# Kernel tuning notes

Measured on AMD Instinct MI355X. Metric: run time of the kernel, lower is better.

Reference implementation:

```python
import jax, jax.numpy as jnp
import numpy as np

D_MODEL = 1024
N_HEADS = 16
D_K = D_MODEL // N_HEADS

def _xavier(key, shape):
    fan_in, fan_out = shape[1], shape[0]
    limit = float(np.sqrt(6.0 / (fan_in + fan_out)))
    return jax.random.uniform(key, shape, jnp.float32, -limit, limit)

def setup_inputs() -> dict:
    key = jax.random.key(0)
    ks = jax.random.split(key, 7)
    B, S = 2, 2048
    return {
        "query": jax.random.normal(ks[0], (B, S, D_MODEL), jnp.float32),
        "key": jax.random.normal(ks[1], (B, S, D_MODEL), jnp.float32),
        "value": jax.random.normal(ks[2], (B, S, D_MODEL), jnp.float32),
        "w_q": _xavier(ks[3], (D_MODEL, D_MODEL)),  # torch Linear weight [out, in]
        "w_k": _xavier(ks[4], (D_MODEL, D_MODEL)),
        "w_v": _xavier(ks[5], (D_MODEL, D_MODEL)),
        "w_o": _xavier(ks[6], (D_MODEL, D_MODEL)),
        "ln_gamma": jnp.ones((D_MODEL,), jnp.float32),
        "ln_beta": jnp.zeros((D_MODEL,), jnp.float32),
    }

def reference(query, key, value, w_q, w_k, w_v, w_o, ln_gamma, ln_beta):
    B, S, _ = query.shape
    # projections (torch Linear: x @ W.T), split into heads -> [B, H, S, d_k]
    def split_heads(x, W):
        return (x @ W.T).reshape(B, S, N_HEADS, D_K).transpose(0, 2, 1, 3)
    Q = split_heads(query, w_q)
    K = split_heads(key, w_k)
    V = split_heads(value, w_v)
    scores = jnp.einsum('bhqd,bhkd->bhqk', Q, K) / jnp.sqrt(jnp.float32(D_K))
    attn = jax.nn.softmax(scores, axis=-1)  # dropout disabled (p=0 / eval)
    ctx = jnp.einsum('bhqk,bhkd->bhqd', attn, V)
    ctx = ctx.transpose(0, 2, 1, 3).reshape(B, S, D_MODEL)
    out = ctx @ w_o.T
    # residual + LayerNorm
    x = query + out
    mu = jnp.mean(x, axis=-1, keepdims=True)
    var = jnp.var(x, axis=-1, keepdims=True)
    return (x - mu) / jnp.sqrt(var + 1e-5) * ln_gamma + ln_beta
```

## Files before the change

### kernel.cpp

```cpp
#include <hip/hip_runtime.h>
#include <hip/hip_bf16.h>

#define DEVI __device__ __forceinline__

typedef float f32x4 __attribute__((ext_vector_type(4)));
typedef short bf16x8 __attribute__((ext_vector_type(8)));
typedef unsigned short ushort_t;

DEVI ushort_t f2bf(float x) {
  union { float f; unsigned u; } c; c.f = x;
  unsigned u = c.u;
  unsigned r = (u + 0x7fffu + ((u >> 16) & 1u)) >> 16;
  return (ushort_t)r;
}

DEVI float bf2f(unsigned hw) {
  union { unsigned u; float f; } c; c.u = hw << 16; return c.f;
}

DEVI unsigned cvt_pk_bf16(float lo, float hi) {
  unsigned r;
  asm volatile("v_cvt_pk_bf16_f32 %0, %1, %2" : "=v"(r) : "v"(lo), "v"(hi));
  return r;
}

DEVI void gload16(const ushort_t* g, ushort_t* l) {
  __builtin_amdgcn_global_load_lds(
      (const __attribute__((address_space(1))) unsigned int*)g,
      (__attribute__((address_space(3))) unsigned int*)l, 16, 0, 0);
}

#define WAITL0() asm volatile("s_waitcnt lgkmcnt(0)" ::: "memory")


__global__ __launch_bounds__(256)
void cvtN_kernel(const float* __restrict__ p0, const float* __restrict__ p1,
                 const float* __restrict__ p2, const float* __restrict__ p3,
                 ushort_t* __restrict__ o0, ushort_t* __restrict__ o1,
                 ushort_t* __restrict__ o2, ushort_t* __restrict__ o3, int n8) {
  int z = blockIdx.y;
  const float* in = (z == 0) ? p0 : (z == 1) ? p1 : (z == 2) ? p2 : p3;
  ushort_t* out = (z == 0) ? o0 : (z == 1) ? o1 : (z == 2) ? o2 : o3;
  int i = blockIdx.x * 256 + threadIdx.x;
  if (i >= n8) return;
  const float4* p = (const float4*)in + (size_t)i * 2;
  float4 a = p[0], b = p[1];
  uint4 v;
  v.x = cvt_pk_bf16(a.x, a.y);
  v.y = cvt_pk_bf16(a.z, a.w);
  v.z = cvt_pk_bf16(b.x, b.y);
  v.w = cvt_pk_bf16(b.z, b.w);
  ((uint4*)out)[i] = v;
}


__global__ __launch_bounds__(256)
void gemm128(const ushort_t* __restrict__ A0, const ushort_t* __restrict__ A1,
             const ushort_t* __restrict__ A2,
             const ushort_t* __restrict__ W0, const ushort_t* __restrict__ W1,
             const ushort_t* __restrict__ W2,
             void* __restrict__ O0, void* __restrict__ O1,
             void* __restrict__ O2, int mode_base, int nsteps, float qscale) {
  constexpr int K = 1024;
  int z = blockIdx.z;
  int mode = (mode_base == 3) ? 3 : mode_base + z;
  const ushort_t* A = (z == 0) ? A0 : (z == 1) ? A1 : A2;
  const ushort_t* W = (z == 0) ? W0 : (z == 1) ? W1 : W2;
  void* Op = (z == 0) ? O0 : (z == 1) ? O1 : O2;
  if (mode == 3) {
    A = A0 + z * 512;
    W = W0 + z * 512;
    Op = z ? O1 : O0;
  }
  float scale = (mode == 0) ? qscale : 1.0f;
  int m0 = (mode == 2) ? blockIdx.x * 128 : blockIdx.y * 128;
  int n0 = (mode == 2) ? blockIdx.y * 128 : blockIdx.x * 128;

  __shared__ __align__(16) ushort_t Asm[2][128 * 64];
  __shared__ __align__(16) ushort_t Bsm[2][128 * 64];

  int t = threadIdx.x;
  int lane = t & 63, wave = t >> 6;
  int wm = wave >> 1, wn = wave & 1;
  int col = lane & 15, g = lane >> 4;
  int lr = lane >> 3, lc = lane & 7;
  int cswz = col & 7;

  const ushort_t* aSrc = A + (size_t)(m0 + wave * 32 + lr) * K + (lc ^ lr) * 8;
  const ushort_t* bSrc = W + (size_t)(n0 + wave * 32 + lr) * K + (lc ^ lr) * 8;

  f32x4 z4 = {0.f, 0.f, 0.f, 0.f};
  f32x4 acc[4][4];
  for (int i = 0; i < 4; i++)
    for (int j = 0; j < 4; j++) acc[i][j] = z4;

#define GEMM_STAGE(buf, koff) do {                                         \
    _Pragma("unroll")                                                      \
    for (int i_ = 0; i_ < 4; i_++) {                                       \
      gload16(aSrc + (koff) + i_ * 8 * K,                                  \
              &Asm[buf][(wave * 32 + i_ * 8) * 64]);                       \
      gload16(bSrc + (koff) + i_ * 8 * K,                                  \
              &Bsm[buf][(wave * 32 + i_ * 8) * 64]);                       \
    }                                                                      \
  } while (0)

  GEMM_STAGE(0, 0);
  __syncthreads();

  for (int kt = 0; kt < nsteps; ++kt) {
    int cur = kt & 1;
    if (kt < nsteps - 1) GEMM_STAGE(cur ^ 1, (kt + 1) * 64);
    const ushort_t* As = Asm[cur];
    const ushort_t* Bs = Bsm[cur];
#pragma unroll
    for (int kk = 0; kk < 2; ++kk) {
      bf16x8 af[4], bfr[4];
#pragma unroll
      for (int mi = 0; mi < 4; mi++) {
        int row = wm * 64 + mi * 16 + col;
        af[mi] = *(const bf16x8*)(As + row * 64 + (((kk * 4 + g) ^ cswz) * 8));
      }
#pragma unroll
      for (int ni = 0; ni < 4; ni++) {
        int row = wn * 64 + ni * 16 + col;
        bfr[ni] = *(const bf16x8*)(Bs + row * 64 + (((kk * 4 + g) ^ cswz) * 8));
      }
      __builtin_amdgcn_s_setprio(1);
#pragma unroll
      for (int mi = 0; mi < 4; mi++)
#pragma unroll
        for (int ni = 0; ni < 4; ni++)
          acc[mi][ni] = __builtin_amdgcn_mfma_f32_16x16x32_bf16(af[mi], bfr[ni],
                                                                acc[mi][ni], 0, 0, 0);
      __builtin_amdgcn_s_setprio(0);
    }
    __syncthreads();
  }

#pragma unroll
  for (int mi = 0; mi < 4; mi++)
#pragma unroll
    for (int ni = 0; ni < 4; ni++)
#pragma unroll
      for (int r = 0; r < 4; r++) {
        int m = m0 + wm * 64 + mi * 16 + g * 4 + r;
        int n = n0 + wn * 64 + ni * 16 + col;
        float v = acc[mi][ni][r] * scale;
        if (mode <= 1) {
          int b = m >> 11, s = m & 2047, h = n >> 6, d = n & 63;
          ((ushort_t*)Op)[(((size_t)(b * 16 + h) * 2048 + s) * 64) + d] = f2bf(v);
        } else if (mode == 2) {
          int h = m >> 6, d = m & 63, b = n >> 11, s = n & 2047;
          ((ushort_t*)Op)[(((size_t)(b * 16 + h) * 64 + d) * 2048) + s] = f2bf(v);
        } else {
          ((ushort_t*)Op)[(size_t)m * 1024 + n] = f2bf(v);
        }
      }
#undef GEMM_STAGE
}


__global__ __launch_bounds__(256, 4)
void attn_kernel(const ushort_t* __restrict__ Qh, const ushort_t* __restrict__ Kh,
                 const ushort_t* __restrict__ Vt, ushort_t* __restrict__ ctx) {
  int qt = blockIdx.x;
  int bh = blockIdx.y;
  int t = threadIdx.x, lane = t & 63, wave = t >> 6;
  int col = lane & 15, g = lane >> 4;
  int lr = lane >> 3, lc = lane & 7;
  int cswz = col & 7;
  int q0 = qt * 128 + wave * 32;

  const ushort_t* Qp = Qh + (size_t)bh * 2048 * 64;
  const ushort_t* Kp = Kh + (size_t)bh * 2048 * 64;
  const ushort_t* Vp = Vt + (size_t)bh * 64 * 2048;

  __shared__ __align__(16) ushort_t Ksm[2][64 * 64];
  __shared__ __align__(16) ushort_t Vsm[2][64 * 64];

  int slot0 = wave * 16 + lr;
  int slot1 = slot0 + 8;
  int key0 = (slot0 & 0x20) | ((slot0 & 0x0C) << 1) | ((slot0 & 0x10) >> 2) | (slot0 & 3);
  int key1 = (slot1 & 0x20) | ((slot1 & 0x0C) << 1) | ((slot1 & 0x10) >> 2) | (slot1 & 3);

  const ushort_t* kSrc0 = Kp + (size_t)key0 * 64 + (lc ^ lr) * 8;
  const ushort_t* kSrc1 = Kp + (size_t)key1 * 64 + (lc ^ lr) * 8;
  const ushort_t* vSrc = Vp + (size_t)(wave * 16 + lr) * 2048 + (lc ^ lr) * 8;

#define ATTN_STAGE(buf, k0) do { \
    gload16(kSrc0 + (size_t)(k0) * 64, &Ksm[buf][wave * 1024]);        \
    gload16(kSrc1 + (size_t)(k0) * 64, &Ksm[buf][wave * 1024 + 512]);  \
    gload16(vSrc + (k0),               &Vsm[buf][wave * 1024]);        \
    gload16(vSrc + (k0) + 16384,       &Vsm[buf][wave * 1024 + 512]);  \
  } while (0)

  bf16x8 qa0 = *(const bf16x8*)(Qp + (size_t)(q0 + col) * 64 + g * 8);
  bf16x8 qa1 = *(const bf16x8*)(Qp + (size_t)(q0 + col) * 64 + 32 + g * 8);
  bf16x8 qb0 = *(const bf16x8*)(Qp + (size_t)(q0 + 16 + col) * 64 + g * 8);
  bf16x8 qb1 = *(const bf16x8*)(Qp + (size_t)(q0 + 16 + col) * 64 + 32 + g * 8);

  f32x4 z4 = {0.f, 0.f, 0.f, 0.f};
  f32x4 oa[4], ob[4];
  for (int i = 0; i < 4; i++) { oa[i] = z4; ob[i] = z4; }
  f32x4 la = z4, lb = z4;

  ATTN_STAGE(0, 0);
  __syncthreads();

  for (int it = 0; it < 32; ++it) {
    int cur = it & 1;
    if (it < 31) ATTN_STAGE(cur ^ 1, (it + 1) * 64);

    const ushort_t* Ks = Ksm[cur];
    const ushort_t* Vs = Vsm[cur];

    f32x4 sa[4], sb[4];
#pragma unroll
    for (int kt = 0; kt < 4; kt++) {
      int off = (kt * 16 + col) * 64 + ((g ^ cswz) * 8);
      bf16x8 kf0 = *(const bf16x8*)(Ks + off);
      bf16x8 kf1 = *(const bf16x8*)(Ks + (off ^ 32));
      f32x4 a = z4, b = z4;
      __builtin_amdgcn_s_setprio(1);
      a = __builtin_amdgcn_mfma_f32_16x16x32_bf16(kf0, qa0, a, 0, 0, 0);
      a = __builtin_amdgcn_mfma_f32_16x16x32_bf16(kf1, qa1, a, 0, 0, 0);
      b = __builtin_amdgcn_mfma_f32_16x16x32_bf16(kf0, qb0, b, 0, 0, 0);
      b = __builtin_amdgcn_mfma_f32_16x16x32_bf16(kf1, qb1, b, 0, 0, 0);
      __builtin_amdgcn_s_setprio(0);
      sa[kt] = a; sb[kt] = b;
    }

    unsigned pka[8], pkb[8];
#pragma unroll
    for (int kt = 0; kt < 4; kt++) {
      float a0 = __builtin_amdgcn_exp2f(sa[kt][0]);
      float a1 = __builtin_amdgcn_exp2f(sa[kt][1]);
      float a2 = __builtin_amdgcn_exp2f(sa[kt][2]);
      float a3 = __builtin_amdgcn_exp2f(sa[kt][3]);
      la[0] += a0; la[1] += a1; la[2] += a2; la[3] += a3;
      pka[2 * kt]     = cvt_pk_bf16(a0, a1);
      pka[2 * kt + 1] = cvt_pk_bf16(a2, a3);
      float b0 = __builtin_amdgcn_exp2f(sb[kt][0]);
      float b1 = __builtin_amdgcn_exp2f(sb[kt][1]);
      float b2 = __builtin_amdgcn_exp2f(sb[kt][2]);
      float b3 = __builtin_amdgcn_exp2f(sb[kt][3]);
      lb[0] += b0; lb[1] += b1; lb[2] += b2; lb[3] += b3;
      pkb[2 * kt]     = cvt_pk_bf16(b0, b1);
      pkb[2 * kt + 1] = cvt_pk_bf16(b2, b3);
    }

#pragma unroll
    for (int kk = 0; kk < 2; kk++) {
      union { uint4 u; bf16x8 f; } ua, ub;
      ua.u.x = pka[4 * kk];     ua.u.y = pka[4 * kk + 1];
      ua.u.z = pka[4 * kk + 2]; ua.u.w = pka[4 * kk + 3];
      ub.u.x = pkb[4 * kk];     ub.u.y = pkb[4 * kk + 1];
      ub.u.z = pkb[4 * kk + 2]; ub.u.w = pkb[4 * kk + 3];
      __builtin_amdgcn_s_setprio(1);
#pragma unroll
      for (int dt = 0; dt < 4; dt++) {
        bf16x8 vf = *(const bf16x8*)(Vs + (dt * 16 + col) * 64 +
                                     (((kk * 4 + g) ^ cswz) * 8));
        oa[dt] = __builtin_amdgcn_mfma_f32_16x16x32_bf16(vf, ua.f, oa[dt], 0, 0, 0);
        ob[dt] = __builtin_amdgcn_mfma_f32_16x16x32_bf16(vf, ub.f, ob[dt], 0, 0, 0);
      }
      __builtin_amdgcn_s_setprio(0);
    }
    __syncthreads();
  }
#undef ATTN_STAGE

  float lva = (la[0] + la[1]) + (la[2] + la[3]);
  lva += __shfl_xor(lva, 16);
  lva += __shfl_xor(lva, 32);
  float lvb = (lb[0] + lb[1]) + (lb[2] + lb[3]);
  lvb += __shfl_xor(lvb, 16);
  lvb += __shfl_xor(lvb, 32);
  float inva = 1.0f / lva, invb = 1.0f / lvb;
  int b = bh >> 4, h = bh & 15;
#pragma unroll
  for (int dt = 0; dt < 4; dt++)
#pragma unroll
    for (int r = 0; r < 4; r++) {
      int d = dt * 16 + g * 4 + r;
      ctx[((size_t)(b * 2048 + q0 + col)) * 1024 + h * 64 + d] =
          f2bf(oa[dt][r] * inva);
      ctx[((size_t)(b * 2048 + q0 + 16 + col)) * 1024 + h * 64 + d] =
          f2bf(ob[dt][r] * invb);
    }
}


__global__ __launch_bounds__(256)
void ln_kernel(const float* __restrict__ resid, const ushort_t* __restrict__ p0,
               const ushort_t* __restrict__ p1,
               const float* __restrict__ gamma, const float* __restrict__ beta,
               float* __restrict__ out) {
  int m = blockIdx.x;
  int t = threadIdx.x;
  int lane = t & 63, wave = t >> 6;
  float4 a = ((const float4*)(resid + (size_t)m * 1024))[t];
  uint2 v0 = ((const uint2*)(p0 + (size_t)m * 1024))[t];
  uint2 v1 = ((const uint2*)(p1 + (size_t)m * 1024))[t];
  float4 x;
  x.x = a.x + bf2f(v0.x & 0xffffu) + bf2f(v1.x & 0xffffu);
  x.y = a.y + bf2f(v0.x >> 16)     + bf2f(v1.x >> 16);
  x.z = a.z + bf2f(v0.y & 0xffffu) + bf2f(v1.y & 0xffffu);
  x.w = a.w + bf2f(v0.y >> 16)     + bf2f(v1.y >> 16);
  float sum = (x.x + x.y) + (x.z + x.w);
  float ssq = x.x * x.x + x.y * x.y + x.z * x.z + x.w * x.w;
  for (int off = 1; off < 64; off <<= 1) {
    sum += __shfl_xor(sum, off);
    ssq += __shfl_xor(ssq, off);
  }
  __shared__ float red[8];
  if (lane == 0) { red[wave] = sum; red[4 + wave] = ssq; }
  __syncthreads();
  sum = red[0] + red[1] + red[2] + red[3];
  ssq = red[4] + red[5] + red[6] + red[7];
  float mu = sum * (1.f / 1024.f);
  float var = ssq * (1.f / 1024.f) - mu * mu;
  float rstd = rsqrtf(var + 1e-5f);
  const float4* gp = (const float4*)gamma;
  const float4* bp = (const float4*)beta;
  float4 gg = gp[t], bb = bp[t];
  float4 y;
  y.x = (x.x - mu) * rstd * gg.x + bb.x;
  y.y = (x.y - mu) * rstd * gg.y + bb.y;
  y.z = (x.z - mu) * rstd * gg.z + bb.z;
  y.w = (x.w - mu) * rstd * gg.w + bb.w;
  ((float4*)(out + (size_t)m * 1024))[t] = y;
}


extern "C" void kernel_launch(void* const* d_in, const int* in_sizes, int n_in,
                              void* d_out, int out_size, void* d_ws, size_t ws_size,
                              hipStream_t stream) {
  (void)in_sizes; (void)n_in; (void)out_size; (void)ws_size;
  const float* query = (const float*)d_in[0];
  const float* keyi  = (const float*)d_in[1];
  const float* value = (const float*)d_in[2];
  const float* w_q = (const float*)d_in[3];
  const float* w_k = (const float*)d_in[4];
  const float* w_v = (const float*)d_in[5];
  const float* w_o = (const float*)d_in[6];
  const float* ln_g = (const float*)d_in[7];
  const float* ln_b = (const float*)d_in[8];

  char* ws = (char*)d_ws;
  const size_t MB = 1u << 20;
  ushort_t* proj0 = (ushort_t*)(ws + 0 * MB);
  ushort_t* proj1 = (ushort_t*)(ws + 8 * MB);
  ushort_t* Xq  = (ushort_t*)(ws + 0 * MB);
  ushort_t* Xk  = (ushort_t*)(ws + 8 * MB);
  ushort_t* Xv  = (ushort_t*)(ws + 16 * MB);
  ushort_t* Wq  = (ushort_t*)(ws + 24 * MB);
  ushort_t* Wk  = (ushort_t*)(ws + 26 * MB);
  ushort_t* Wv  = (ushort_t*)(ws + 28 * MB);
  ushort_t* Wo  = (ushort_t*)(ws + 30 * MB);
  ushort_t* Qh  = (ushort_t*)(ws + 32 * MB);
  ushort_t* Kh  = (ushort_t*)(ws + 40 * MB);
  ushort_t* Vt  = (ushort_t*)(ws + 48 * MB);
  ushort_t* ctx = (ushort_t*)(ws + 56 * MB);

  const float SCL = 0.18033688f;

  cvtN_kernel<<<dim3(2048, 3), 256, 0, stream>>>(query, keyi, value, value,
                                                 Xq, Xk, Xv, Xv, 524288);
  cvtN_kernel<<<dim3(512, 4), 256, 0, stream>>>(w_q, w_k, w_v, w_o,
                                                Wq, Wk, Wv, Wo, 131072);

  gemm128<<<dim3(8, 32, 3), 256, 0, stream>>>(Xq, Xk, Wv, Wq, Wk, Xv,
                                              Qh, Kh, Vt, 0, 16, SCL);
  attn_kernel<<<dim3(16, 32), 256, 0, stream>>>(Qh, Kh, Vt, ctx);
  gemm128<<<dim3(8, 32, 2), 256, 0, stream>>>(ctx, ctx, ctx, Wo, Wo, Wo,
                                              proj0, proj1, proj0, 3, 8, 1.0f);
  ln_kernel<<<4096, 256, 0, stream>>>(query, proj0, proj1, ln_g, ln_b,
                                      (float*)d_out);
}
```

Measured before the change: 140.2 us.

## Split attention over two key halves with a reduce kernel; merge conversion launches

The attention kernel now splits the 2048 keys into two halves along a new grid z dimension. Each half writes unnormalized bf16 partial outputs and fp32 row sums, and a new reduce kernel adds them and normalizes into ctx. This doubles the number of attention blocks so more CUs and occupancy slots are used. The cost is an extra launch, extra memory traffic for the partials, and bf16 rounding of unnormalized partials. Merging the partials by plain addition is only correct if the softmax uses no per-half running max, which depends on code not shown. The two fp32-to-bf16 conversion launches are also folded into one kernel.

```diff
diff --git a/kernel.cpp b/kernel.cpp
--- a/kernel.cpp
+++ b/kernel.cpp
@@ -34,15 +34,28 @@
 
 
 __global__ __launch_bounds__(256)
-void cvtN_kernel(const float* __restrict__ p0, const float* __restrict__ p1,
-                 const float* __restrict__ p2, const float* __restrict__ p3,
-                 ushort_t* __restrict__ o0, ushort_t* __restrict__ o1,
-                 ushort_t* __restrict__ o2, ushort_t* __restrict__ o3, int n8) {
+void cvt_all_kernel(const float* __restrict__ p0, const float* __restrict__ p1,
+                    const float* __restrict__ p2,
+                    const float* __restrict__ w0, const float* __restrict__ w1,
+                    const float* __restrict__ w2, const float* __restrict__ w3,
+                    ushort_t* __restrict__ o0, ushort_t* __restrict__ o1,
+                    ushort_t* __restrict__ o2,
+                    ushort_t* __restrict__ q0, ushort_t* __restrict__ q1,
+                    ushort_t* __restrict__ q2, ushort_t* __restrict__ q3) {
   int z = blockIdx.y;
-  const float* in = (z == 0) ? p0 : (z == 1) ? p1 : (z == 2) ? p2 : p3;
-  ushort_t* out = (z == 0) ? o0 : (z == 1) ? o1 : (z == 2) ? o2 : o3;
   int i = blockIdx.x * 256 + threadIdx.x;
-  if (i >= n8) return;
+  const float* in;
+  ushort_t* out;
+  if (z < 3) {
+    in = (z == 0) ? p0 : (z == 1) ? p1 : p2;
+    out = (z == 0) ? o0 : (z == 1) ? o1 : o2;
+  } else {
+    int w = i >> 17;
+    int local = i & 131071;
+    in = ((w == 0) ? w0 : (w == 1) ? w1 : (w == 2) ? w2 : w3);
+    out = ((w == 0) ? q0 : (w == 1) ? q1 : (w == 2) ? q2 : q3);
+    i = local;
+  }
   const float4* p = (const float4*)in + (size_t)i * 2;
   float4 a = p[0], b = p[1];
   uint4 v;
@@ -162,14 +175,20 @@
 
 __global__ __launch_bounds__(256, 4)
 void attn_kernel(const ushort_t* __restrict__ Qh, const ushort_t* __restrict__ Kh,
-                 const ushort_t* __restrict__ Vt, ushort_t* __restrict__ ctx) {
+                 const ushort_t* __restrict__ Vt,
+                 ushort_t* __restrict__ op0, ushort_t* __restrict__ op1,
+                 float* __restrict__ lp0, float* __restrict__ lp1) {
   int qt = blockIdx.x;
   int bh = blockIdx.y;
+  int sp = blockIdx.z;
   int t = threadIdx.x, lane = t & 63, wave = t >> 6;
   int col = lane & 15, g = lane >> 4;
   int lr = lane >> 3, lc = lane & 7;
   int cswz = col & 7;
   int q0 = qt * 128 + wave * 32;
+  int kbase = sp * 1024;
+  ushort_t* opart = sp ? op1 : op0;
+  float* lpart = sp ? lp1 : lp0;
 
   const ushort_t* Qp = Qh + (size_t)bh * 2048 * 64;
   const ushort_t* Kp = Kh + (size_t)bh * 2048 * 64;
@@ -204,12 +223,13 @@
   for (int i = 0; i < 4; i++) { oa[i] = z4; ob[i] = z4; }
   f32x4 la = z4, lb = z4;
 
-  ATTN_STAGE(0, 0);
+  ATTN_STAGE(0, kbase);
   __syncthreads();
 
-  for (int it = 0; it < 32; ++it) {
+  for (int it = 0; it < 16; ++it) {
     int cur = it & 1;
-    if (it < 31) ATTN_STAGE(cur ^ 1, (it + 1) * 64);
+    int k0 = kbase + it * 64;
+    if (it < 15) ATTN_STAGE(cur ^ 1, k0 + 64);
 
     const ushort_t* Ks = Ksm[cur];
     const ushort_t* Vs = Vsm[cur];
@@ -276,18 +296,44 @@
   float lvb = (lb[0] + lb[1]) + (lb[2] + lb[3]);
   lvb += __shfl_xor(lvb, 16);
   lvb += __shfl_xor(lvb, 32);
-  float inva = 1.0f / lva, invb = 1.0f / lvb;
+  if (g == 0) {
+    lpart[(size_t)bh * 2048 + q0 + col] = lva;
+    lpart[(size_t)bh * 2048 + q0 + 16 + col] = lvb;
+  }
   int b = bh >> 4, h = bh & 15;
 #pragma unroll
   for (int dt = 0; dt < 4; dt++)
 #pragma unroll
     for (int r = 0; r < 4; r++) {
       int d = dt * 16 + g * 4 + r;
-      ctx[((size_t)(b * 2048 + q0 + col)) * 1024 + h * 64 + d] =
-          f2bf(oa[dt][r] * inva);
-      ctx[((size_t)(b * 2048 + q0 + 16 + col)) * 1024 + h * 64 + d] =
-          f2bf(ob[dt][r] * invb);
+      opart[((size_t)(b * 2048 + q0 + col)) * 1024 + h * 64 + d] =
+          f2bf(oa[dt][r]);
+      opart[((size_t)(b * 2048 + q0 + 16 + col)) * 1024 + h * 64 + d] =
+          f2bf(ob[dt][r]);
     }
+}
+
+
+__global__ __launch_bounds__(256)
+void attn_reduce(const ushort_t* __restrict__ o0, const ushort_t* __restrict__ o1,
+                 const float* __restrict__ l0, const float* __restrict__ l1,
+                 ushort_t* __restrict__ ctx) {
+  int m = blockIdx.x;
+  int t = threadIdx.x;
+  int b = m >> 11, q = m & 2047;
+  int h = t >> 4;
+  size_t li = (size_t)(b * 16 + h) * 2048 + q;
+  float inv = 1.0f / (l0[li] + l1[li]);
+  uint2 a = ((const uint2*)(o0 + (size_t)m * 1024))[t];
+  uint2 c = ((const uint2*)(o1 + (size_t)m * 1024))[t];
+  float x0 = (bf2f(a.x & 0xffffu) + bf2f(c.x & 0xffffu)) * inv;
+  float x1 = (bf2f(a.x >> 16)     + bf2f(c.x >> 16))     * inv;
+  float x2 = (bf2f(a.y & 0xffffu) + bf2f(c.y & 0xffffu)) * inv;
+  float x3 = (bf2f(a.y >> 16)     + bf2f(c.y >> 16))     * inv;
+  uint2 o;
+  o.x = cvt_pk_bf16(x0, x1);
+  o.y = cvt_pk_bf16(x2, x3);
+  ((uint2*)(ctx + (size_t)m * 1024))[t] = o;
 }
 
 
@@ -349,11 +395,15 @@
 
   char* ws = (char*)d_ws;
   const size_t MB = 1u << 20;
-  ushort_t* proj0 = (ushort_t*)(ws + 0 * MB);
-  ushort_t* proj1 = (ushort_t*)(ws + 8 * MB);
   ushort_t* Xq  = (ushort_t*)(ws + 0 * MB);
   ushort_t* Xk  = (ushort_t*)(ws + 8 * MB);
   ushort_t* Xv  = (ushort_t*)(ws + 16 * MB);
+  ushort_t* op0 = (ushort_t*)(ws + 0 * MB);
+  ushort_t* op1 = (ushort_t*)(ws + 8 * MB);
+  float*    l0  = (float*)   (ws + 16 * MB);
+  float*    l1  = (float*)   (ws + 17 * MB);
+  ushort_t* proj0 = (ushort_t*)(ws + 0 * MB);
+  ushort_t* proj1 = (ushort_t*)(ws + 8 * MB);
   ushort_t* Wq  = (ushort_t*)(ws + 24 * MB);
   ushort_t* Wk  = (ushort_t*)(ws + 26 * MB);
   ushort_t* Wv  = (ushort_t*)(ws + 28 * MB);
@@ -365,14 +415,15 @@
 
   const float SCL = 0.18033688f;
 
-  cvtN_kernel<<<dim3(2048, 3), 256, 0, stream>>>(query, keyi, value, value,
-                                                 Xq, Xk, Xv, Xv, 524288);
-  cvtN_kernel<<<dim3(512, 4), 256, 0, stream>>>(w_q, w_k, w_v, w_o,
-                                                Wq, Wk, Wv, Wo, 131072);
+  cvt_all_kernel<<<dim3(2048, 4), 256, 0, stream>>>(
+      query, keyi, value, w_q, w_k, w_v, w_o,
+      Xq, Xk, Xv, Wq, Wk, Wv, Wo);
 
   gemm128<<<dim3(8, 32, 3), 256, 0, stream>>>(Xq, Xk, Wv, Wq, Wk, Xv,
                                               Qh, Kh, Vt, 0, 16, SCL);
-  attn_kernel<<<dim3(16, 32), 256, 0, stream>>>(Qh, Kh, Vt, ctx);
+  attn_kernel<<<dim3(16, 32, 2), 256, 0, stream>>>(Qh, Kh, Vt,
+                                                   op0, op1, l0, l1);
+  attn_reduce<<<4096, 256, 0, stream>>>(op0, op1, l0, l1, ctx);
   gemm128<<<dim3(8, 32, 2), 256, 0, stream>>>(ctx, ctx, ctx, Wo, Wo, Wo,
                                               proj0, proj1, proj0, 3, 8, 1.0f);
   ln_kernel<<<4096, 256, 0, stream>>>(query, proj0, proj1, ln_g, ln_b,
```

Measured after the change: 140.8 us. No clear change (+0.4%).
